# Kernel optimization log

Hardware: AMD Instinct MI355X
Metric: run time of the kernel (lower is better)

## Reference

```python
import jax, jax.numpy as jnp
import numpy as np

Q = 1          # hard-coded in the original forward
LAM = 1e-3     # ridge regularizer of the ELM-AE least-squares solve


def setup_inputs() -> dict:
    key = jax.random.key(0)
    k1, k2 = jax.random.split(key)
    B, Z, H, W = 64, 512, 32, 32
    x = jax.random.normal(k1, (B, Z, H, W), dtype=jnp.float32)
    # fixed random ELM hidden-layer weights (Q x z); the repo generates these
    # with a deterministic LCG, here plain gaussian random
    Wh = jax.random.normal(k2, (Q, Z), dtype=jnp.float32)
    return {"x": x, "W": Wh}


def reference(x, W):
    # x: [B, Z, h, w]  -> per-sample feature matrix X: [Z, N] with N = h*w pixels
    B, Z, h, w = x.shape
    X = x.reshape(B, Z, h * w)                      # [B, Z, N]
    # ELM-AE: random hidden activations over pixels
    Hh = jax.nn.sigmoid(jnp.einsum('qz,bzn->bqn', W, X))   # [B, Q, N]
    G = jnp.einsum('bqn,bpn->bqp', Hh, Hh) + LAM * jnp.eye(Q, dtype=x.dtype)  # [B, Q, Q]
    XHt = jnp.einsum('bzn,bqn->bzq', X, Hh)         # [B, Z, Q]
    # solve G^T Beta^T = XHt^T  (G symmetric)
    Beta = jnp.swapaxes(jnp.linalg.solve(G, jnp.swapaxes(XHt, 1, 2)), 1, 2)  # [B, Z, Q]
    # pooled features flattened to (B, Q*Z, 1) as in the original
    out = Beta.reshape(B, Q * Z, 1)
    return out
```

## Files before the change

kernel.cpp:

```cpp
#include <hip/hip_runtime.h>
#include <hip/hip_bf16.h>

#define B_ 64
#define Z_ 512
#define N_ 1024
#define LAM 1e-3f
#define NQ 16
#define NR 64
#define NTL 2
#define TH 1024

__global__ __launch_bounds__(TH) void elm_k1(
    const float* __restrict__ x, const float* __restrict__ Wh,
    float* __restrict__ out, float* __restrict__ gws) {
  __shared__ float part[16][NR];
  __shared__ float h_lds[NR];

  const int t   = threadIdx.x;
  const int bid = blockIdx.x;
  const int b   = bid >> 4;
  const int nq  = bid & 15;
  const int nbase = nq * NR;
  const size_t xb = (size_t)b * (size_t)(Z_ * N_);
  const int jg = t & 7;
  const int zr = t >> 3;
  const int wv = t >> 6;
  const int ln = t & 63;

  float4 v[NTL][4];
#pragma unroll
  for (int tl = 0; tl < NTL; ++tl)
#pragma unroll
    for (int k = 0; k < 4; ++k)
      v[tl][k] = *reinterpret_cast<const float4*>(
          x + xb + (size_t)(zr + 128 * k) * N_ + (nbase + tl * 32 + jg * 4));

  float w[4];
#pragma unroll
  for (int k = 0; k < 4; ++k) w[k] = Wh[zr + 128 * k];

  float sp[NTL][4];
#pragma unroll
  for (int tl = 0; tl < NTL; ++tl)
#pragma unroll
    for (int i = 0; i < 4; ++i) {
      const float* vp0 = reinterpret_cast<const float*>(&v[tl][0]);
      const float* vp1 = reinterpret_cast<const float*>(&v[tl][1]);
      const float* vp2 = reinterpret_cast<const float*>(&v[tl][2]);
      const float* vp3 = reinterpret_cast<const float*>(&v[tl][3]);
      sp[tl][i] = w[0] * vp0[i] + w[1] * vp1[i] + w[2] * vp2[i] + w[3] * vp3[i];
    }
#pragma unroll
  for (int tl = 0; tl < NTL; ++tl)
#pragma unroll
    for (int i = 0; i < 4; ++i) {
      float s = sp[tl][i];
      s += __shfl_xor(s, 8);
      s += __shfl_xor(s, 16);
      s += __shfl_xor(s, 32);
      sp[tl][i] = s;
    }
  if (ln < 8) {
#pragma unroll
    for (int tl = 0; tl < NTL; ++tl)
#pragma unroll
      for (int i = 0; i < 4; ++i)
        part[wv][tl * 32 + ln * 4 + i] = sp[tl][i];
  }
  __syncthreads();

  if (t < NR) {
    float s = 0.f;
#pragma unroll
    for (int w16 = 0; w16 < 16; ++w16) s += part[w16][t];
    const float h = 1.f / (1.f + __expf(-s));
    h_lds[t] = h;
    float q = h * h;
    q += __shfl_xor(q, 1);
    q += __shfl_xor(q, 2);
    q += __shfl_xor(q, 4);
    q += __shfl_xor(q, 8);
    q += __shfl_xor(q, 16);
    q += __shfl_xor(q, 32);
    if (t == 0) gws[bid] = q;
  }
  __syncthreads();

  float acc[4] = {0.f, 0.f, 0.f, 0.f};
#pragma unroll
  for (int tl = 0; tl < NTL; ++tl)
#pragma unroll
    for (int i = 0; i < 4; ++i) {
      const float h = h_lds[tl * 32 + jg * 4 + i];
      const float* vp0 = reinterpret_cast<const float*>(&v[tl][0]);
      const float* vp1 = reinterpret_cast<const float*>(&v[tl][1]);
      const float* vp2 = reinterpret_cast<const float*>(&v[tl][2]);
      const float* vp3 = reinterpret_cast<const float*>(&v[tl][3]);
      acc[0] += h * vp0[i];
      acc[1] += h * vp1[i];
      acc[2] += h * vp2[i];
      acc[3] += h * vp3[i];
    }
#pragma unroll
  for (int k = 0; k < 4; ++k) {
    float a = acc[k];
    a += __shfl_xor(a, 1);
    a += __shfl_xor(a, 2);
    a += __shfl_xor(a, 4);
    if (jg == 0) atomicAdd(&out[b * Z_ + zr + 128 * k], a);
  }
}

__global__ void elm_k2(float* __restrict__ out, const float* __restrict__ gws) {
  const int b = blockIdx.x;
  __shared__ float ginv;
  if (threadIdx.x == 0) {
    float g = LAM;
#pragma unroll
    for (int i = 0; i < NQ; ++i) g += gws[b * NQ + i];
    ginv = 1.f / g;
  }
  __syncthreads();
  out[b * Z_ + threadIdx.x] *= ginv;
}

extern "C" void kernel_launch(void* const* d_in, const int* in_sizes, int n_in,
                              void* d_out, int out_size, void* d_ws, size_t ws_size,
                              hipStream_t stream) {
  const float* x  = (const float*)d_in[0];
  const float* Wh = (const float*)d_in[1];
  float* out = (float*)d_out;
  float* gws = (float*)d_ws;

  hipMemsetAsync(out, 0, (size_t)B_ * Z_ * sizeof(float), stream);
  elm_k1<<<dim3(B_ * NQ), dim3(TH), 0, stream>>>(x, Wh, out, gws);
  elm_k2<<<dim3(B_), dim3(Z_), 0, stream>>>(out, gws);
}
```

Before: 33.62 us.

## Replace atomic accumulation with per-block partials reduced in second kernel

Each block of the main kernel now handles 32 pixels with 512 threads instead of 64 pixels with 1024 threads, so twice as many smaller blocks cover the work. Instead of atomically adding per-block X·H^T contributions into the output, each block writes its partial vector to workspace, and the finalize kernel sums the 32 partials per sample and applies the 1/(G+lam) scale. This removes the memset launch and the atomic contention on the output. The cost is an extra 4 MB workspace write and read, plus a wave-level shuffle reduction of the G partials.

```diff
diff --git a/kernel.cpp b/kernel.cpp
--- a/kernel.cpp
+++ b/kernel.cpp
@@ -5,74 +5,58 @@
 #define Z_ 512
 #define N_ 1024
 #define LAM 1e-3f
-#define NQ 16
-#define NR 64
-#define NTL 2
-#define TH 1024
+#define NQ 32
+#define NC 32
+#define TH 512
+#define WS_XH (B_ * NQ * Z_)
 
-__global__ __launch_bounds__(TH) void elm_k1(
+__global__ __launch_bounds__(TH, 8) void elm_k1(
     const float* __restrict__ x, const float* __restrict__ Wh,
-    float* __restrict__ out, float* __restrict__ gws) {
-  __shared__ float part[16][NR];
-  __shared__ float h_lds[NR];
+    float* __restrict__ pxh, float* __restrict__ gws) {
+  __shared__ float part[8][NC];
+  __shared__ float h_lds[NC];
 
   const int t   = threadIdx.x;
   const int bid = blockIdx.x;
-  const int b   = bid >> 4;
-  const int nq  = bid & 15;
-  const int nbase = nq * NR;
-  const size_t xb = (size_t)b * (size_t)(Z_ * N_);
-  const int jg = t & 7;
-  const int zr = t >> 3;
-  const int wv = t >> 6;
-  const int ln = t & 63;
+  const int b   = bid >> 5;
+  const int nq  = bid & 31;
+  const int jg  = t & 7;
+  const int zr  = t >> 3;
+  const int wv  = t >> 6;
+  const int ln  = t & 63;
 
-  float4 v[NTL][4];
+  const float* xp = x + (size_t)b * (Z_ * N_) + (size_t)zr * N_ + (nq * NC + jg * 4);
+
+  float4 v[8];
 #pragma unroll
-  for (int tl = 0; tl < NTL; ++tl)
+  for (int k = 0; k < 8; ++k)
+    v[k] = *reinterpret_cast<const float4*>(xp + (size_t)(64 * k) * N_);
+
+  float w[8];
 #pragma unroll
-    for (int k = 0; k < 4; ++k)
-      v[tl][k] = *reinterpret_cast<const float4*>(
-          x + xb + (size_t)(zr + 128 * k) * N_ + (nbase + tl * 32 + jg * 4));
+  for (int k = 0; k < 8; ++k) w[k] = Wh[zr + 64 * k];
 
-  float w[4];
+  float sp[4];
 #pragma unroll
-  for (int k = 0; k < 4; ++k) w[k] = Wh[zr + 128 * k];
-
-  float sp[NTL][4];
+  for (int i = 0; i < 4; ++i) {
+    float s = 0.f;
 #pragma unroll
-  for (int tl = 0; tl < NTL; ++tl)
-#pragma unroll
-    for (int i = 0; i < 4; ++i) {
-      const float* vp0 = reinterpret_cast<const float*>(&v[tl][0]);
-      const float* vp1 = reinterpret_cast<const float*>(&v[tl][1]);
-      const float* vp2 = reinterpret_cast<const float*>(&v[tl][2]);
-      const float* vp3 = reinterpret_cast<const float*>(&v[tl][3]);
-      sp[tl][i] = w[0] * vp0[i] + w[1] * vp1[i] + w[2] * vp2[i] + w[3] * vp3[i];
-    }
-#pragma unroll
-  for (int tl = 0; tl < NTL; ++tl)
-#pragma unroll
-    for (int i = 0; i < 4; ++i) {
-      float s = sp[tl][i];
-      s += __shfl_xor(s, 8);
-      s += __shfl_xor(s, 16);
-      s += __shfl_xor(s, 32);
-      sp[tl][i] = s;
-    }
+    for (int k = 0; k < 8; ++k) s += w[k] * reinterpret_cast<const float*>(&v[k])[i];
+    s += __shfl_xor(s, 8);
+    s += __shfl_xor(s, 16);
+    s += __shfl_xor(s, 32);
+    sp[i] = s;
+  }
   if (ln < 8) {
 #pragma unroll
-    for (int tl = 0; tl < NTL; ++tl)
-#pragma unroll
-      for (int i = 0; i < 4; ++i)
-        part[wv][tl * 32 + ln * 4 + i] = sp[tl][i];
+    for (int i = 0; i < 4; ++i) part[wv][ln * 4 + i] = sp[i];
   }
   __syncthreads();
 
-  if (t < NR) {
+  if (t < NC) {
     float s = 0.f;
 #pragma unroll
-    for (int w16 = 0; w16 < 16; ++w16) s += part[w16][t];
+    for (int w8 = 0; w8 < 8; ++w8) s += part[w8][t];
     const float h = 1.f / (1.f + __expf(-s));
     h_lds[t] = h;
     float q = h * h;
@@ -81,47 +65,47 @@
     q += __shfl_xor(q, 4);
     q += __shfl_xor(q, 8);
     q += __shfl_xor(q, 16);
-    q += __shfl_xor(q, 32);
     if (t == 0) gws[bid] = q;
   }
   __syncthreads();
 
-  float acc[4] = {0.f, 0.f, 0.f, 0.f};
+  float acc[8] = {0.f, 0.f, 0.f, 0.f, 0.f, 0.f, 0.f, 0.f};
 #pragma unroll
-  for (int tl = 0; tl < NTL; ++tl)
+  for (int i = 0; i < 4; ++i) {
+    const float h = h_lds[jg * 4 + i];
 #pragma unroll
-    for (int i = 0; i < 4; ++i) {
-      const float h = h_lds[tl * 32 + jg * 4 + i];
-      const float* vp0 = reinterpret_cast<const float*>(&v[tl][0]);
-      const float* vp1 = reinterpret_cast<const float*>(&v[tl][1]);
-      const float* vp2 = reinterpret_cast<const float*>(&v[tl][2]);
-      const float* vp3 = reinterpret_cast<const float*>(&v[tl][3]);
-      acc[0] += h * vp0[i];
-      acc[1] += h * vp1[i];
-      acc[2] += h * vp2[i];
-      acc[3] += h * vp3[i];
-    }
+    for (int k = 0; k < 8; ++k) acc[k] += h * reinterpret_cast<const float*>(&v[k])[i];
+  }
 #pragma unroll
-  for (int k = 0; k < 4; ++k) {
+  for (int k = 0; k < 8; ++k) {
     float a = acc[k];
     a += __shfl_xor(a, 1);
     a += __shfl_xor(a, 2);
     a += __shfl_xor(a, 4);
-    if (jg == 0) atomicAdd(&out[b * Z_ + zr + 128 * k], a);
+    if (jg == 0) pxh[(size_t)bid * Z_ + zr + 64 * k] = a;
   }
 }
 
-__global__ void elm_k2(float* __restrict__ out, const float* __restrict__ gws) {
+__global__ __launch_bounds__(Z_) void elm_k2(
+    const float* __restrict__ pxh, const float* __restrict__ gws,
+    float* __restrict__ out) {
   const int b = blockIdx.x;
+  const int t = threadIdx.x;
   __shared__ float ginv;
-  if (threadIdx.x == 0) {
-    float g = LAM;
-#pragma unroll
-    for (int i = 0; i < NQ; ++i) g += gws[b * NQ + i];
-    ginv = 1.f / g;
+  if (t < 32) {
+    float g = gws[b * NQ + t];
+    g += __shfl_xor(g, 1);
+    g += __shfl_xor(g, 2);
+    g += __shfl_xor(g, 4);
+    g += __shfl_xor(g, 8);
+    g += __shfl_xor(g, 16);
+    if (t == 0) ginv = 1.f / (g + LAM);
   }
   __syncthreads();
-  out[b * Z_ + threadIdx.x] *= ginv;
+  float s = 0.f;
+#pragma unroll
+  for (int nq = 0; nq < NQ; ++nq) s += pxh[((size_t)b * NQ + nq) * Z_ + t];
+  out[b * Z_ + t] = s * ginv;
 }
 
 extern "C" void kernel_launch(void* const* d_in, const int* in_sizes, int n_in,
@@ -130,9 +114,9 @@
   const float* x  = (const float*)d_in[0];
   const float* Wh = (const float*)d_in[1];
   float* out = (float*)d_out;
-  float* gws = (float*)d_ws;
+  float* pxh = (float*)d_ws;
+  float* gws = (float*)d_ws + WS_XH;
 
-  hipMemsetAsync(out, 0, (size_t)B_ * Z_ * sizeof(float), stream);
-  elm_k1<<<dim3(B_ * NQ), dim3(TH), 0, stream>>>(x, Wh, out, gws);
-  elm_k2<<<dim3(B_), dim3(Z_), 0, stream>>>(out, gws);
+  elm_k1<<<dim3(B_ * NQ), dim3(TH), 0, stream>>>(x, Wh, pxh, gws);
+  elm_k2<<<dim3(B_), dim3(Z_), 0, stream>>>(pxh, gws, out);
 }
```

Result: faster. 30.89 us (-8.1%).
